# Performance work log

Measured on AMD Instinct MI355X. Metric: run time of the kernel, lower is better.

## Reference

```python
import jax, jax.numpy as jnp
import numpy as np

HEADS = 12
LN_EPS = 1e-5


def setup_inputs() -> dict:
    B, S, D = 2, 2048, 768
    k = jax.random.key(0)
    ks = jax.random.split(k, 16)
    std = 0.02
    inp = {
        "key": jax.random.normal(ks[0], (B, S, D), jnp.float32),
        "query": jax.random.normal(ks[1], (B, S, D), jnp.float32),
        "value": jax.random.normal(ks[2], (B, S, D), jnp.float32),
        "mask": jax.random.randint(ks[3], (B, S, S), 0, 2).astype(bool),
        "Wk_w": jax.random.normal(ks[4], (D, D), jnp.float32) * std,
        "Wk_b": jnp.zeros((D,), jnp.float32),
        "Wq_w": jax.random.normal(ks[5], (D, D), jnp.float32) * std,
        "Wq_b": jnp.zeros((D,), jnp.float32),
        "Wv_w": jax.random.normal(ks[6], (D, D), jnp.float32) * std,
        "Wv_b": jnp.zeros((D,), jnp.float32),
        "Wc_w": jax.random.normal(ks[7], (D, D), jnp.float32) * std,
        "Wc_b": jnp.zeros((D,), jnp.float32),
        "ln_g": jnp.ones((D,), jnp.float32),
        "ln_b": jnp.zeros((D,), jnp.float32),
    }
    return inp


def _mha(key, query, value, mask, Wk_w, Wk_b, Wq_w, Wq_b, Wv_w, Wv_b,
         Wc_w, Wc_b, ln_g, ln_b):
    B, Sq, D = query.shape
    Sk = key.shape[1]
    H = HEADS
    hd = D // H
    scaler = np.float32(D ** 0.5)  # NOTE: source scales by sqrt(hidden_size), not sqrt(head_dim)

    # QKV projections (torch Linear: x @ W.T + b)
    hk = (key @ Wk_w.T + Wk_b).reshape(B, Sk, H, hd).transpose(2, 0, 1, 3)    # (H,B,Sk,hd)
    hq = (query @ Wq_w.T + Wq_b).reshape(B, Sq, H, hd).transpose(2, 0, 1, 3)  # (H,B,Sq,hd)
    hv = (value @ Wv_w.T + Wv_b).reshape(B, Sk, H, hd).transpose(2, 0, 1, 3)  # (H,B,Sk,hd)

    qk = jnp.einsum('hbqd,hbkd->hbqk', hq, hk) / scaler
    qk = jnp.where(mask[None], -jnp.inf, qk)  # mask repeated over heads in source
    attn = jax.nn.softmax(qk, axis=-1)        # dropout is identity in eval
    out = jnp.einsum('hbqk,hbkd->hbqd', attn, hv)  # (H,B,Sq,hd)

    # Faithful replication of source reshape chain:
    # (H*B,Sq,hd).view(B,H,Sq,hd).permute(1,2,0,3).view(B,Sq,D)
    out = out.reshape(B, H, Sq, hd)             # flat reinterpretation, head-major data
    out = jnp.transpose(out, (1, 2, 0, 3)).reshape(B, Sq, D)

    out = out @ Wc_w.T + Wc_b                   # Wconcat; dropout identity
    x = out + query                             # residual
    mu = jnp.mean(x, axis=-1, keepdims=True)
    var = jnp.mean((x - mu) ** 2, axis=-1, keepdims=True)
    return ln_g * (x - mu) / jnp.sqrt(var + LN_EPS) + ln_b


def reference(key, query, value, mask, Wk_w, Wk_b, Wq_w, Wq_b, Wv_w, Wv_b,
              Wc_w, Wc_b, ln_g, ln_b):
    return _mha(key, query, value, mask, Wk_w, Wk_b, Wq_w, Wq_b,
                Wv_w, Wv_b, Wc_w, Wc_b, ln_g, ln_b)
```

## Files before the change

### kernel.cpp

```cpp
#include <hip/hip_runtime.h>
#include <stdint.h>

typedef float v4f __attribute__((ext_vector_type(4)));
typedef short v8s __attribute__((ext_vector_type(8)));

#define AS1 __attribute__((address_space(1)))
#define AS3 __attribute__((address_space(3)))

__device__ __forceinline__ void load16_to_lds(const void* g, void* l) {
  __builtin_amdgcn_global_load_lds((AS1 void*)g, (AS3 void*)l, 16, 0, 0);
}
__device__ __forceinline__ void load4_to_lds(const void* g, void* l) {
  __builtin_amdgcn_global_load_lds((AS1 void*)g, (AS3 void*)l, 4, 0, 0);
}

__device__ __forceinline__ float fexp2(float x) {
#if __has_builtin(__builtin_amdgcn_exp2f)
  return __builtin_amdgcn_exp2f(x);
#else
  return exp2f(x);
#endif
}

__device__ __forceinline__ unsigned short f2bf_rn(float f) {
  union { float f; uint32_t u; } v; v.f = f;
  return (unsigned short)((v.u + 0x8000u) >> 16);
}
__device__ __forceinline__ uint32_t pack_bf2(float x, float y) {
  union { float f; uint32_t u; } a, b; a.f = x; b.f = y;
  return __builtin_amdgcn_perm(b.u + 0x8000u, a.u + 0x8000u, 0x07060302u);
}

#define QSCALE 0.052058786f

__global__ __launch_bounds__(256) void pack_mask_kernel(
    const uint32_t* __restrict__ mask, uint32_t* __restrict__ bits) {
  __shared__ int s_i32;
  const int tid = threadIdx.x;
  if (tid == 0) s_i32 = 1;
  __syncthreads();
  if (mask[tid] > 1u) s_i32 = 0;
  __syncthreads();
  if (s_i32) {
    const int lane = tid & 63;
    const int gw = (blockIdx.x * 256 + tid) >> 6;
#pragma unroll 4
    for (int it = 0; it < 32; ++it) {
      const size_t base = (size_t)gw * 2048 + it * 64;
      unsigned long long bal = __ballot(mask[base + lane] != 0u);
      if (lane == 0) *(unsigned long long*)&bits[base >> 5] = bal;
    }
  } else {
    const int wi = blockIdx.x * 256 + tid;
    const uint32_t* p = mask + (size_t)wi * 8;
    uint32_t w = 0;
#pragma unroll
    for (int j8 = 0; j8 < 8; ++j8) {
      uint32_t u = p[j8];
#pragma unroll
      for (int k = 0; k < 4; ++k)
        w |= (((u >> (8 * k)) & 0xFFu) ? 1u : 0u) << (j8 * 4 + k);
    }
    bits[wi] = w;
  }
}

__global__ __launch_bounds__(256) void conv_kernel(
    const float* __restrict__ wk, const float* __restrict__ wq,
    const float* __restrict__ wv, const float* __restrict__ wc,
    const float* __restrict__ kin, const float* __restrict__ qin,
    const float* __restrict__ vin,
    unsigned short* __restrict__ dk, unsigned short* __restrict__ dq,
    unsigned short* __restrict__ dv, unsigned short* __restrict__ dc,
    unsigned short* __restrict__ dki, unsigned short* __restrict__ dqi,
    unsigned short* __restrict__ dvi) {
  const int y = blockIdx.y;
  const float* s; unsigned short* d; float sc = 1.f; int n4;
  switch (y) {
    case 0: s = wk;  d = dk;  n4 = 147456; break;
    case 1: s = wq;  d = dq;  n4 = 147456; sc = QSCALE; break;
    case 2: s = wv;  d = dv;  n4 = 147456; break;
    case 3: s = wc;  d = dc;  n4 = 147456; break;
    case 4: s = kin; d = dki; n4 = 786432; break;
    case 5: s = qin; d = dqi; n4 = 786432; break;
    default: s = vin; d = dvi; n4 = 786432; break;
  }
  const int i = blockIdx.x * 256 + threadIdx.x;
  if (i >= n4) return;
  float4 f = ((const float4*)s)[i];
  uint2 o;
  o.x = pack_bf2(f.x * sc, f.y * sc);
  o.y = pack_bf2(f.z * sc, f.w * sc);
  ((uint2*)d)[i] = o;
}

__global__ __launch_bounds__(256, 3) void gemm_qkv_kernel(
    const unsigned short* __restrict__ qin, const unsigned short* __restrict__ kin,
    const unsigned short* __restrict__ vin,
    const unsigned short* __restrict__ wqb, const unsigned short* __restrict__ wkb,
    const unsigned short* __restrict__ wvb,
    const float* __restrict__ bq, const float* __restrict__ bk,
    const float* __restrict__ bv,
    unsigned short* __restrict__ Qb, unsigned short* __restrict__ Kb,
    unsigned short* __restrict__ Vt) {
  const int which = blockIdx.z;
  const unsigned short* A; const unsigned short* Wb; const float* bias;
  float bscale = 1.f;
  if (which == 0)      { A = qin; Wb = wqb; bias = bq; bscale = QSCALE; }
  else if (which == 1) { A = kin; Wb = wkb; bias = bk; }
  else                 { A = vin; Wb = wvb; bias = bv; }

  const int m0 = blockIdx.x * 128, n0 = blockIdx.y * 128;
  const int tid = threadIdx.x, lane = tid & 63, wid = tid >> 6;
  const int wm = wid >> 1, wn = wid & 1;
  const int l16 = lane & 15, quad = lane >> 4;

  __shared__ __align__(16) unsigned short As[2][128 * 32];
  __shared__ __align__(16) unsigned short Bs[2][128 * 32];

  v4f acc[4][4];
#pragma unroll
  for (int i = 0; i < 4; ++i)
#pragma unroll
    for (int j = 0; j < 4; ++j) { v4f z = {0.f, 0.f, 0.f, 0.f}; acc[i][j] = z; }

  const int c0 = wid * 128 + lane, c1 = wid * 128 + 64 + lane;
  const unsigned short* a0 = A + (size_t)(m0 + (c0 >> 2)) * 768 + (c0 & 3) * 8;
  const unsigned short* a1 = A + (size_t)(m0 + (c1 >> 2)) * 768 + (c1 & 3) * 8;
  const unsigned short* b0 = Wb + (size_t)(n0 + (c0 >> 2)) * 768 + (c0 & 3) * 8;
  const unsigned short* b1 = Wb + (size_t)(n0 + (c1 >> 2)) * 768 + (c1 & 3) * 8;

#define QKV_STAGE(k0, buf)                                         \
  do {                                                             \
    load16_to_lds(a0 + (k0), &As[buf][(wid * 128) * 8]);           \
    load16_to_lds(a1 + (k0), &As[buf][(wid * 128 + 64) * 8]);      \
    load16_to_lds(b0 + (k0), &Bs[buf][(wid * 128) * 8]);           \
    load16_to_lds(b1 + (k0), &Bs[buf][(wid * 128 + 64) * 8]);      \
  } while (0)

  QKV_STAGE(0, 0);
#pragma unroll 2
  for (int ks = 0; ks < 24; ++ks) {
    const int bufc = ks & 1;
    __syncthreads();
    v8s af[4], bf[4];
#pragma unroll
    for (int i = 0; i < 4; ++i)
      af[i] = *(const v8s*)&As[bufc][(wm * 64 + i * 16 + l16) * 32 + quad * 8];
#pragma unroll
    for (int j = 0; j < 4; ++j)
      bf[j] = *(const v8s*)&Bs[bufc][(wn * 64 + j * 16 + l16) * 32 + quad * 8];
    if (ks < 23) QKV_STAGE((ks + 1) * 32, bufc ^ 1);
#pragma unroll
    for (int i = 0; i < 4; ++i)
#pragma unroll
      for (int j = 0; j < 4; ++j)
        acc[i][j] = __builtin_amdgcn_mfma_f32_16x16x32_bf16(af[i], bf[j],
                                                            acc[i][j], 0, 0, 0);
  }
#undef QKV_STAGE

#pragma unroll
  for (int i = 0; i < 4; ++i) {
#pragma unroll
    for (int j = 0; j < 4; ++j) {
      const int mbase = m0 + wm * 64 + i * 16 + quad * 4;
      const int n = n0 + wn * 64 + j * 16 + l16;
      const float bv_ = bias[n] * bscale;
      if (which == 2) {
        const int bb = mbase >> 11, ss = mbase & 2047;
        uint2 pk;
        pk.x = pack_bf2(acc[i][j][0] + bv_, acc[i][j][1] + bv_);
        pk.y = pack_bf2(acc[i][j][2] + bv_, acc[i][j][3] + bv_);
        *(uint2*)&Vt[((size_t)bb * 768 + n) * 2048 + ss] = pk;
      } else {
        unsigned short* dst = (which == 0) ? Qb : Kb;
#pragma unroll
        for (int r = 0; r < 4; ++r)
          dst[(size_t)(mbase + r) * 768 + n] = f2bf_rn(acc[i][j][r] + bv_);
      }
    }
  }
}

__global__ __launch_bounds__(256, 3) void attn_kernel(
    const unsigned short* __restrict__ Qb, const unsigned short* __restrict__ Kb,
    const unsigned short* __restrict__ Vt, const uint32_t* __restrict__ mbits,
    unsigned short* __restrict__ X) {
  const int q0 = blockIdx.x * 64;
  const int h = blockIdx.y, b = blockIdx.z;
  const int tid = threadIdx.x, w = tid >> 6, lane = tid & 63;
  const int l16 = lane & 15, quad = lane >> 4, l7 = l16 & 7;

  __shared__ __align__(16) unsigned short Kl[2][64 * 64];
  __shared__ __align__(16) unsigned short Vl[2][64 * 64];
  __shared__ __align__(16) unsigned short Pl[4][16 * 64];
  __shared__ uint32_t Ml[2][128];

  v8s aq[2];
  {
    const unsigned short* qp =
        Qb + (size_t)(b * 2048 + q0 + w * 16 + l16) * 768 + h * 64 + quad * 8;
    aq[0] = *(const v8s*)qp;
    aq[1] = *(const v8s*)(qp + 32);
  }

  v4f o[4], ol;
#pragma unroll
  for (int nt = 0; nt < 4; ++nt) { v4f z = {0.f, 0.f, 0.f, 0.f}; o[nt] = z; }
  { v4f z = {0.f, 0.f, 0.f, 0.f}; ol = z; }

  v8s bones;
  {
    const short v1 = (l16 == 0) ? (short)0x3F80 : (short)0;
#pragma unroll
    for (int j = 0; j < 8; ++j) bones[j] = v1;
  }

  const int rsub = lane >> 3;
  const int csub = ((lane & 7) ^ rsub) * 8;
  const unsigned short* kg0 = Kb + (size_t)(b * 2048 + w * 16) * 768 + h * 64;
  const unsigned short* vg0 = Vt + (size_t)(b * 768 + h * 64 + w * 16) * 2048;
  const uint32_t* mg0 =
      mbits + (size_t)(b * 2048 + q0 + w * 32 + (lane >> 1)) * 64 + (lane & 1);

#define ATTN_STAGE(kk0, buf)                                                  \
  do {                                                                        \
    const unsigned short* kg = kg0 + (size_t)(kk0) * 768;                     \
    const unsigned short* vg = vg0 + (kk0);                                   \
    load16_to_lds(kg + (size_t)rsub * 768 + csub, &Kl[buf][(w * 16) * 64]);   \
    load16_to_lds(kg + (size_t)(8 + rsub) * 768 + csub,                       \
                  &Kl[buf][(w * 16 + 8) * 64]);                               \
    load16_to_lds(vg + (size_t)rsub * 2048 + csub, &Vl[buf][(w * 16) * 64]);  \
    load16_to_lds(vg + (size_t)(8 + rsub) * 2048 + csub,                      \
                  &Vl[buf][(w * 16 + 8) * 64]);                               \
    if (w < 2) load4_to_lds(mg0 + ((kk0) >> 5), &Ml[buf][w * 64]);            \
  } while (0)

  ATTN_STAGE(0, 0);
#pragma unroll 2
  for (int it = 0; it < 32; ++it) {
    const int bufc = it & 1;
    __syncthreads();

    v8s bk[2][4];
#pragma unroll
    for (int kt = 0; kt < 2; ++kt)
#pragma unroll
      for (int nt = 0; nt < 4; ++nt)
        bk[kt][nt] = *(const v8s*)&Kl[bufc][(nt * 16 + l16) * 64 +
                                           (((kt * 4 + quad) ^ l7) << 3)];
    if (it < 31) ATTN_STAGE((it + 1) * 64, bufc ^ 1);

    v4f sacc[4];
#pragma unroll
    for (int nt = 0; nt < 4; ++nt) { v4f z = {0.f, 0.f, 0.f, 0.f}; sacc[nt] = z; }
#pragma unroll
    for (int kt = 0; kt < 2; ++kt)
#pragma unroll
      for (int nt = 0; nt < 4; ++nt)
        sacc[nt] = __builtin_amdgcn_mfma_f32_16x16x32_bf16(aq[kt], bk[kt][nt],
                                                           sacc[nt], 0, 0, 0);

    const int rowb = w * 16 + quad * 4;
    const int hi = l16 >> 3;
#pragma unroll
    for (int r = 0; r < 4; ++r) {
      const uint2 mw = *(const uint2*)&Ml[bufc][(rowb + r - w * 16 + w * 16) * 2];
      const uint32_t u0 = mw.x >> l16, u1 = mw.y >> l16;
      const float p0 = (u0 & 1u) ? 0.f : fexp2(sacc[0][r]);
      const float p1 = ((u0 >> 16) & 1u) ? 0.f : fexp2(sacc[1][r]);
      const float p2 = (u1 & 1u) ? 0.f : fexp2(sacc[2][r]);
      const float p3 = ((u1 >> 16) & 1u) ? 0.f : fexp2(sacc[3][r]);
      const int prow = quad * 4 + r, ps = prow & 7;
      const int base = prow * 64 + l7;
      Pl[w][base + (((0 + hi) ^ ps) << 3)] = f2bf_rn(p0);
      Pl[w][base + (((2 + hi) ^ ps) << 3)] = f2bf_rn(p1);
      Pl[w][base + (((4 + hi) ^ ps) << 3)] = f2bf_rn(p2);
      Pl[w][base + (((6 + hi) ^ ps) << 3)] = f2bf_rn(p3);
    }

#pragma unroll
    for (int kt = 0; kt < 2; ++kt) {
      const v8s ap = *(const v8s*)&Pl[w][l16 * 64 + (((kt * 4 + quad) ^ l7) << 3)];
#pragma unroll
      for (int nt = 0; nt < 4; ++nt) {
        const v8s bv = *(const v8s*)&Vl[bufc][(nt * 16 + l16) * 64 +
                                             (((kt * 4 + quad) ^ l7) << 3)];
        o[nt] = __builtin_amdgcn_mfma_f32_16x16x32_bf16(ap, bv, o[nt], 0, 0, 0);
      }
      ol = __builtin_amdgcn_mfma_f32_16x16x32_bf16(ap, bones, ol, 0, 0, 0);
    }
  }
#undef ATTN_STAGE

  const int hb2 = 2 * h + b;
  const int b2 = (hb2 >= 12) ? 1 : 0;
  const int h2 = hb2 - 12 * b2;
#pragma unroll
  for (int r = 0; r < 4; ++r) {
    const float lsum = __shfl(ol[r], quad * 16, 64);
    const float inv_l = 1.f / lsum;
    const int q = q0 + w * 16 + quad * 4 + r;
#pragma unroll
    for (int nt = 0; nt < 4; ++nt) {
      const int d = nt * 16 + l16;
      const size_t f = (size_t)h2 * 262144 + (size_t)q * 128 + b2 * 64 + d;
      X[f] = f2bf_rn(o[nt][r] * inv_l);
    }
  }
}

__global__ __launch_bounds__(256, 3) void gemm2_kernel(
    const unsigned short* __restrict__ X, const unsigned short* __restrict__ Wcb,
    const float* __restrict__ bc, const float* __restrict__ query,
    float* __restrict__ out) {
  const int m0 = blockIdx.x * 64, n0 = blockIdx.y * 128;
  const int tid = threadIdx.x, lane = tid & 63, wid = tid >> 6;
  const int wm = wid >> 1, wn = wid & 1;
  const int l16 = lane & 15, quad = lane >> 4;

  __shared__ __align__(16) unsigned short As[2][64 * 32];
  __shared__ __align__(16) unsigned short Bs[2][128 * 32];

  v4f acc[2][4];
#pragma unroll
  for (int i = 0; i < 2; ++i)
#pragma unroll
    for (int j = 0; j < 4; ++j) { v4f z = {0.f, 0.f, 0.f, 0.f}; acc[i][j] = z; }

  const int ca = tid;
  const unsigned short* a0 = X + (size_t)(m0 + (ca >> 2)) * 768 + (ca & 3) * 8;
  const int c0 = wid * 128 + lane, c1 = wid * 128 + 64 + lane;
  const unsigned short* b0 = Wcb + (size_t)(n0 + (c0 >> 2)) * 768 + (c0 & 3) * 8;
  const unsigned short* b1 = Wcb + (size_t)(n0 + (c1 >> 2)) * 768 + (c1 & 3) * 8;

#define G2_STAGE(k0, buf)                                        \
  do {                                                           \
    load16_to_lds(a0 + (k0), &As[buf][(wid * 64) * 8]);          \
    load16_to_lds(b0 + (k0), &Bs[buf][(wid * 128) * 8]);         \
    load16_to_lds(b1 + (k0), &Bs[buf][(wid * 128 + 64) * 8]);    \
  } while (0)

  G2_STAGE(0, 0);
#pragma unroll 2
  for (int ks = 0; ks < 24; ++ks) {
    const int bufc = ks & 1;
    __syncthreads();
    v8s af[2], bf[4];
#pragma unroll
    for (int i = 0; i < 2; ++i)
      af[i] = *(const v8s*)&As[bufc][(wm * 32 + i * 16 + l16) * 32 + quad * 8];
#pragma unroll
    for (int j = 0; j < 4; ++j)
      bf[j] = *(const v8s*)&Bs[bufc][(wn * 64 + j * 16 + l16) * 32 + quad * 8];
    if (ks < 23) G2_STAGE((ks + 1) * 32, bufc ^ 1);
#pragma unroll
    for (int i = 0; i < 2; ++i)
#pragma unroll
      for (int j = 0; j < 4; ++j)
        acc[i][j] = __builtin_amdgcn_mfma_f32_16x16x32_bf16(af[i], bf[j],
                                                            acc[i][j], 0, 0, 0);
  }
#undef G2_STAGE

#pragma unroll
  for (int i = 0; i < 2; ++i) {
#pragma unroll
    for (int j = 0; j < 4; ++j) {
      const int mbase = m0 + wm * 32 + i * 16 + quad * 4;
      const int n = n0 + wn * 64 + j * 16 + l16;
      const float bv_ = bc[n];
#pragma unroll
      for (int r = 0; r < 4; ++r) {
        const int m = mbase + r;
        out[(size_t)m * 768 + n] =
            acc[i][j][r] + bv_ + query[(size_t)m * 768 + n];
      }
    }
  }
}

__global__ __launch_bounds__(256) void ln_kernel(float* __restrict__ out,
                                                 const float* __restrict__ g,
                                                 const float* __restrict__ bta) {
  const int row = blockIdx.x;
  const int tid = threadIdx.x;
  float x[3];
  float s = 0.f, sq = 0.f;
#pragma unroll
  for (int k = 0; k < 3; ++k) {
    x[k] = out[(size_t)row * 768 + tid + k * 256];
    s += x[k];
    sq += x[k] * x[k];
  }
#pragma unroll
  for (int off = 1; off < 64; off <<= 1) {
    s += __shfl_xor(s, off, 64);
    sq += __shfl_xor(sq, off, 64);
  }
  __shared__ float ss[4], ssq[4];
  const int w = tid >> 6, lane = tid & 63;
  if (lane == 0) { ss[w] = s; ssq[w] = sq; }
  __syncthreads();
  s = ss[0] + ss[1] + ss[2] + ss[3];
  sq = ssq[0] + ssq[1] + ssq[2] + ssq[3];
  const float mu = s * (1.f / 768.f);
  const float var = sq * (1.f / 768.f) - mu * mu;
  const float rstd = rsqrtf(var + 1e-5f);
#pragma unroll
  for (int k = 0; k < 3; ++k) {
    const int cc = tid + k * 256;
    out[(size_t)row * 768 + cc] = g[cc] * (x[k] - mu) * rstd + bta[cc];
  }
}

extern "C" void kernel_launch(void* const* d_in, const int* in_sizes, int n_in,
                              void* d_out, int out_size, void* d_ws,
                              size_t ws_size, hipStream_t stream) {
  const float* key   = (const float*)d_in[0];
  const float* query = (const float*)d_in[1];
  const float* value = (const float*)d_in[2];
  const uint32_t* mask = (const uint32_t*)d_in[3];
  const float* Wk = (const float*)d_in[4];
  const float* bk = (const float*)d_in[5];
  const float* Wq = (const float*)d_in[6];
  const float* bq = (const float*)d_in[7];
  const float* Wv = (const float*)d_in[8];
  const float* bv = (const float*)d_in[9];
  const float* Wc = (const float*)d_in[10];
  const float* bc = (const float*)d_in[11];
  const float* lng = (const float*)d_in[12];
  const float* lnb = (const float*)d_in[13];

  char* ws = (char*)d_ws;
  uint32_t*       mbits = (uint32_t*)(ws);
  unsigned short* Wkb = (unsigned short*)(ws + 0x100000);
  unsigned short* Wqb = (unsigned short*)(ws + 0x220000);
  unsigned short* Wvb = (unsigned short*)(ws + 0x340000);
  unsigned short* Wcb = (unsigned short*)(ws + 0x460000);
  unsigned short* Qb  = (unsigned short*)(ws + 0x600000);
  unsigned short* Kb  = (unsigned short*)(ws + 0xC00000);
  unsigned short* Vt  = (unsigned short*)(ws + 0x1200000);
  unsigned short* X   = (unsigned short*)(ws + 0x1800000);
  unsigned short* Kin = (unsigned short*)d_out;
  unsigned short* Qin = (unsigned short*)d_out + 3145728;
  unsigned short* Vin = X;
  float* out = (float*)d_out;

  pack_mask_kernel<<<dim3(1024), dim3(256), 0, stream>>>(mask, mbits);
  conv_kernel<<<dim3(3072, 7), dim3(256), 0, stream>>>(
      Wk, Wq, Wv, Wc, key, query, value,
      Wkb, Wqb, Wvb, Wcb, Kin, Qin, Vin);
  gemm_qkv_kernel<<<dim3(32, 6, 3), dim3(256), 0, stream>>>(
      Qin, Kin, Vin, Wqb, Wkb, Wvb, bq, bk, bv, Qb, Kb, Vt);
  attn_kernel<<<dim3(32, 12, 2), dim3(256), 0, stream>>>(Qb, Kb, Vt, mbits, X);
  gemm2_kernel<<<dim3(64, 6), dim3(256), 0, stream>>>(X, Wcb, bc, query, out);
  ln_kernel<<<dim3(4096), dim3(256), 0, stream>>>(out, lng, lnb);
}
```

Before: 243.9 us.

## Fuse mask packing into conv kernel and transpose QK^T MFMA for register-held mask

Merges the mask bit-packing kernel into the bf16 conversion kernel as extra blocks in a compact 1D grid, which removes one launch and the idle blocks of the old 3072x7 grid. In attention, the QK^T MFMA operands are swapped so each lane holds a transposed score tile. Mask bits are then loaded per row into registers with one-iteration prefetch instead of staged through LDS. P is written to LDS as packed 8-byte stores, and launch bounds rise to 4 waves per SIMD, which risks register pressure or spills.

```diff
diff --git a/kernel.cpp b/kernel.cpp
--- a/kernel.cpp
+++ b/kernel.cpp
@@ -9,9 +9,6 @@
 
 __device__ __forceinline__ void load16_to_lds(const void* g, void* l) {
   __builtin_amdgcn_global_load_lds((AS1 void*)g, (AS3 void*)l, 16, 0, 0);
-}
-__device__ __forceinline__ void load4_to_lds(const void* g, void* l) {
-  __builtin_amdgcn_global_load_lds((AS1 void*)g, (AS3 void*)l, 4, 0, 0);
 }
 
 __device__ __forceinline__ float fexp2(float x) {
@@ -33,60 +30,65 @@
 
 #define QSCALE 0.052058786f
 
-__global__ __launch_bounds__(256) void pack_mask_kernel(
-    const uint32_t* __restrict__ mask, uint32_t* __restrict__ bits) {
-  __shared__ int s_i32;
-  const int tid = threadIdx.x;
-  if (tid == 0) s_i32 = 1;
-  __syncthreads();
-  if (mask[tid] > 1u) s_i32 = 0;
-  __syncthreads();
-  if (s_i32) {
-    const int lane = tid & 63;
-    const int gw = (blockIdx.x * 256 + tid) >> 6;
-#pragma unroll 4
-    for (int it = 0; it < 32; ++it) {
-      const size_t base = (size_t)gw * 2048 + it * 64;
-      unsigned long long bal = __ballot(mask[base + lane] != 0u);
-      if (lane == 0) *(unsigned long long*)&bits[base >> 5] = bal;
-    }
-  } else {
-    const int wi = blockIdx.x * 256 + tid;
-    const uint32_t* p = mask + (size_t)wi * 8;
-    uint32_t w = 0;
-#pragma unroll
-    for (int j8 = 0; j8 < 8; ++j8) {
-      uint32_t u = p[j8];
-#pragma unroll
-      for (int k = 0; k < 4; ++k)
-        w |= (((u >> (8 * k)) & 0xFFu) ? 1u : 0u) << (j8 * 4 + k);
-    }
-    bits[wi] = w;
-  }
-}
-
-__global__ __launch_bounds__(256) void conv_kernel(
+__global__ __launch_bounds__(256) void conv_pack_kernel(
     const float* __restrict__ wk, const float* __restrict__ wq,
     const float* __restrict__ wv, const float* __restrict__ wc,
     const float* __restrict__ kin, const float* __restrict__ qin,
-    const float* __restrict__ vin,
+    const float* __restrict__ vin, const uint32_t* __restrict__ mask,
     unsigned short* __restrict__ dk, unsigned short* __restrict__ dq,
     unsigned short* __restrict__ dv, unsigned short* __restrict__ dc,
     unsigned short* __restrict__ dki, unsigned short* __restrict__ dqi,
-    unsigned short* __restrict__ dvi) {
-  const int y = blockIdx.y;
-  const float* s; unsigned short* d; float sc = 1.f; int n4;
-  switch (y) {
-    case 0: s = wk;  d = dk;  n4 = 147456; break;
-    case 1: s = wq;  d = dq;  n4 = 147456; sc = QSCALE; break;
-    case 2: s = wv;  d = dv;  n4 = 147456; break;
-    case 3: s = wc;  d = dc;  n4 = 147456; break;
-    case 4: s = kin; d = dki; n4 = 786432; break;
-    case 5: s = qin; d = dqi; n4 = 786432; break;
-    default: s = vin; d = dvi; n4 = 786432; break;
-  }
-  const int i = blockIdx.x * 256 + threadIdx.x;
-  if (i >= n4) return;
+    unsigned short* __restrict__ dvi, uint32_t* __restrict__ bits) {
+  const int id = blockIdx.x;
+  const int tid = threadIdx.x;
+  if (id >= 11520) {
+    const int xx = id - 11520;
+    __shared__ int s_i32;
+    if (tid == 0) s_i32 = 1;
+    __syncthreads();
+    if (mask[tid] > 1u) s_i32 = 0;
+    __syncthreads();
+    if (s_i32) {
+      const int lane = tid & 63;
+      const int gw = (xx * 256 + tid) >> 6;
+#pragma unroll 4
+      for (int it = 0; it < 32; ++it) {
+        const size_t base = (size_t)gw * 2048 + it * 64;
+        unsigned long long bal = __ballot(mask[base + lane] != 0u);
+        if (lane == 0) *(unsigned long long*)&bits[base >> 5] = bal;
+      }
+    } else {
+      const int wi = xx * 256 + tid;
+      const uint32_t* p = mask + (size_t)wi * 8;
+      uint32_t w = 0;
+#pragma unroll
+      for (int j8 = 0; j8 < 8; ++j8) {
+        uint32_t u = p[j8];
+#pragma unroll
+        for (int k = 0; k < 4; ++k)
+          w |= (((u >> (8 * k)) & 0xFFu) ? 1u : 0u) << (j8 * 4 + k);
+      }
+      bits[wi] = w;
+    }
+    return;
+  }
+  const float* s; unsigned short* d; float sc = 1.f; int x;
+  if (id < 2304) {
+    const int y = id / 576;
+    x = id - y * 576;
+    if (y == 0)      { s = wk; d = dk; }
+    else if (y == 1) { s = wq; d = dq; sc = QSCALE; }
+    else if (y == 2) { s = wv; d = dv; }
+    else             { s = wc; d = dc; }
+  } else {
+    const int t = id - 2304;
+    const int y = t / 3072;
+    x = t - y * 3072;
+    if (y == 0)      { s = kin; d = dki; }
+    else if (y == 1) { s = qin; d = dqi; }
+    else             { s = vin; d = dvi; }
+  }
+  const int i = x * 256 + tid;
   float4 f = ((const float4*)s)[i];
   uint2 o;
   o.x = pack_bf2(f.x * sc, f.y * sc);
@@ -183,7 +185,7 @@
   }
 }
 
-__global__ __launch_bounds__(256, 3) void attn_kernel(
+__global__ __launch_bounds__(256, 4) void attn_kernel(
     const unsigned short* __restrict__ Qb, const unsigned short* __restrict__ Kb,
     const unsigned short* __restrict__ Vt, const uint32_t* __restrict__ mbits,
     unsigned short* __restrict__ X) {
@@ -195,7 +197,6 @@
   __shared__ __align__(16) unsigned short Kl[2][64 * 64];
   __shared__ __align__(16) unsigned short Vl[2][64 * 64];
   __shared__ __align__(16) unsigned short Pl[4][16 * 64];
-  __shared__ uint32_t Ml[2][128];
 
   v8s aq[2];
   {
@@ -221,23 +222,23 @@
   const int csub = ((lane & 7) ^ rsub) * 8;
   const unsigned short* kg0 = Kb + (size_t)(b * 2048 + w * 16) * 768 + h * 64;
   const unsigned short* vg0 = Vt + (size_t)(b * 768 + h * 64 + w * 16) * 2048;
-  const uint32_t* mg0 =
-      mbits + (size_t)(b * 2048 + q0 + w * 32 + (lane >> 1)) * 64 + (lane & 1);
-
-#define ATTN_STAGE(kk0, buf)                                                  \
-  do {                                                                        \
-    const unsigned short* kg = kg0 + (size_t)(kk0) * 768;                     \
-    const unsigned short* vg = vg0 + (kk0);                                   \
-    load16_to_lds(kg + (size_t)rsub * 768 + csub, &Kl[buf][(w * 16) * 64]);   \
-    load16_to_lds(kg + (size_t)(8 + rsub) * 768 + csub,                       \
-                  &Kl[buf][(w * 16 + 8) * 64]);                               \
-    load16_to_lds(vg + (size_t)rsub * 2048 + csub, &Vl[buf][(w * 16) * 64]);  \
-    load16_to_lds(vg + (size_t)(8 + rsub) * 2048 + csub,                      \
-                  &Vl[buf][(w * 16 + 8) * 64]);                               \
-    if (w < 2) load4_to_lds(mg0 + ((kk0) >> 5), &Ml[buf][w * 64]);            \
+  const uint2* mp =
+      (const uint2*)(mbits + (size_t)(b * 2048 + q0 + w * 16 + l16) * 64);
+
+#define ATTN_STAGE(kk0, buf)                                                   \
+  do {                                                                         \
+    const unsigned short* kg = kg0 + (size_t)(kk0) * 768;                      \
+    const unsigned short* vg = vg0 + (kk0);                                    \
+    load16_to_lds(kg + (size_t)rsub * 768 + csub, &Kl[buf][(w * 16) * 64]);    \
+    load16_to_lds(kg + (size_t)(8 + rsub) * 768 + csub,                        \
+                  &Kl[buf][(w * 16 + 8) * 64]);                                \
+    load16_to_lds(vg + (size_t)rsub * 2048 + csub, &Vl[buf][(w * 16) * 64]);   \
+    load16_to_lds(vg + (size_t)(8 + rsub) * 2048 + csub,                       \
+                  &Vl[buf][(w * 16 + 8) * 64]);                                \
   } while (0)
 
   ATTN_STAGE(0, 0);
+  uint2 mreg = mp[0];
 #pragma unroll 2
   for (int it = 0; it < 32; ++it) {
     const int bufc = it & 1;
@@ -250,7 +251,11 @@
       for (int nt = 0; nt < 4; ++nt)
         bk[kt][nt] = *(const v8s*)&Kl[bufc][(nt * 16 + l16) * 64 +
                                            (((kt * 4 + quad) ^ l7) << 3)];
-    if (it < 31) ATTN_STAGE((it + 1) * 64, bufc ^ 1);
+    uint2 mnext;
+    if (it < 31) {
+      ATTN_STAGE((it + 1) * 64, bufc ^ 1);
+      mnext = mp[it + 1];
+    }
 
     v4f sacc[4];
 #pragma unroll
@@ -259,25 +264,23 @@
     for (int kt = 0; kt < 2; ++kt)
 #pragma unroll
       for (int nt = 0; nt < 4; ++nt)
-        sacc[nt] = __builtin_amdgcn_mfma_f32_16x16x32_bf16(aq[kt], bk[kt][nt],
+        sacc[nt] = __builtin_amdgcn_mfma_f32_16x16x32_bf16(bk[kt][nt], aq[kt],
                                                            sacc[nt], 0, 0, 0);
 
-    const int rowb = w * 16 + quad * 4;
-    const int hi = l16 >> 3;
-#pragma unroll
-    for (int r = 0; r < 4; ++r) {
-      const uint2 mw = *(const uint2*)&Ml[bufc][(rowb + r - w * 16 + w * 16) * 2];
-      const uint32_t u0 = mw.x >> l16, u1 = mw.y >> l16;
-      const float p0 = (u0 & 1u) ? 0.f : fexp2(sacc[0][r]);
-      const float p1 = ((u0 >> 16) & 1u) ? 0.f : fexp2(sacc[1][r]);
-      const float p2 = (u1 & 1u) ? 0.f : fexp2(sacc[2][r]);
-      const float p3 = ((u1 >> 16) & 1u) ? 0.f : fexp2(sacc[3][r]);
-      const int prow = quad * 4 + r, ps = prow & 7;
-      const int base = prow * 64 + l7;
-      Pl[w][base + (((0 + hi) ^ ps) << 3)] = f2bf_rn(p0);
-      Pl[w][base + (((2 + hi) ^ ps) << 3)] = f2bf_rn(p1);
-      Pl[w][base + (((4 + hi) ^ ps) << 3)] = f2bf_rn(p2);
-      Pl[w][base + (((6 + hi) ^ ps) << 3)] = f2bf_rn(p3);
+    const uint32_t u[4] = {mreg.x >> (quad * 4), mreg.x >> (quad * 4 + 16),
+                           mreg.y >> (quad * 4), mreg.y >> (quad * 4 + 16)};
+#pragma unroll
+    for (int nt = 0; nt < 4; ++nt) {
+      const float p0 = (u[nt] & 1u) ? 0.f : fexp2(sacc[nt][0]);
+      const float p1 = ((u[nt] >> 1) & 1u) ? 0.f : fexp2(sacc[nt][1]);
+      const float p2 = ((u[nt] >> 2) & 1u) ? 0.f : fexp2(sacc[nt][2]);
+      const float p3 = ((u[nt] >> 3) & 1u) ? 0.f : fexp2(sacc[nt][3]);
+      uint2 pk;
+      pk.x = pack_bf2(p0, p1);
+      pk.y = pack_bf2(p2, p3);
+      const int elem =
+          l16 * 64 + (((nt * 2 + (quad >> 1)) ^ l7) << 3) + (quad & 1) * 4;
+      *(uint2*)&Pl[w][elem] = pk;
     }
 
 #pragma unroll
@@ -291,6 +294,7 @@
       }
       ol = __builtin_amdgcn_mfma_f32_16x16x32_bf16(ap, bones, ol, 0, 0, 0);
     }
+    mreg = mnext;
   }
 #undef ATTN_STAGE
 
@@ -448,10 +452,9 @@
   unsigned short* Vin = X;
   float* out = (float*)d_out;
 
-  pack_mask_kernel<<<dim3(1024), dim3(256), 0, stream>>>(mask, mbits);
-  conv_kernel<<<dim3(3072, 7), dim3(256), 0, stream>>>(
-      Wk, Wq, Wv, Wc, key, query, value,
-      Wkb, Wqb, Wvb, Wcb, Kin, Qin, Vin);
+  conv_pack_kernel<<<dim3(12544), dim3(256), 0, stream>>>(
+      Wk, Wq, Wv, Wc, key, query, value, mask,
+      Wkb, Wqb, Wvb, Wcb, Kin, Qin, Vin, mbits);
   gemm_qkv_kernel<<<dim3(32, 6, 3), dim3(256), 0, stream>>>(
       Qin, Kin, Vin, Wqb, Wkb, Wvb, bq, bk, bv, Qb, Kb, Vt);
   attn_kernel<<<dim3(32, 12, 2), dim3(256), 0, stream>>>(Qb, Kb, Vt, mbits, X);
```

After: 241.2 us. Within noise of the previous version (-1.1%).
